# Performance work log

Hardware: AMD Instinct MI355X
Metric: run time of the kernel (lower is better)

Reference implementation:

```python
import jax, jax.numpy as jnp
import numpy as np

B, H, S, D = 2, 16, 2048, 64

def setup_inputs() -> dict:
    key = jax.random.key(0)
    kq, kk, kv = jax.random.split(key, 3)
    query = jax.random.normal(kq, (B, H, S, D), dtype=jnp.float32)
    k_ = jax.random.normal(kk, (B, H, S, D), dtype=jnp.float32)
    value = jax.random.normal(kv, (B, H, S, D), dtype=jnp.float32)
    # causal bool mask: True = masked (matches torch masked_fill semantics)
    attn_mask = jnp.triu(jnp.ones((S, S), dtype=bool), k=1)
    # no padding (all False) so no softmax row is fully masked
    key_padding_mask = jnp.zeros((B, S), dtype=bool)
    return {"query": query, "key": k_, "value": value,
            "attn_mask": attn_mask, "key_padding_mask": key_padding_mask}

def reference(query, key, value, attn_mask, key_padding_mask):
    scale = query.shape[-1] ** -0.5
    # [B,H,Sq,Sk] scores
    scores = jnp.einsum('bhqd,bhkd->bhqk', query, key) * scale
    scores = jnp.where(key_padding_mask[:, None, None, :], -jnp.inf, scores)
    scores = jnp.where(attn_mask, -jnp.inf, scores)
    attn = jax.nn.softmax(scores, axis=-1)
    # dropout=0.0 -> identity in eval/math
    return jnp.einsum('bhqk,bhkd->bhqd', attn, value)
```

## Files before the change

### kernel.cpp

```cpp
#include <hip/hip_runtime.h>
#include <hip/hip_bf16.h>


#define BHN 32
#define SEQ 2048
#define DIM 64
#define LSTR 72

typedef __attribute__((ext_vector_type(8)))  short    short8;
typedef __attribute__((ext_vector_type(4)))  short    short4v;
typedef __attribute__((ext_vector_type(4)))  float    float4v;
typedef __attribute__((ext_vector_type(16))) float    f32x16;
typedef __attribute__((ext_vector_type(4)))  unsigned uint4v;

__device__ __forceinline__ short f2b(float x) {
  __hip_bfloat16 h = __float2bfloat16(x);
  return __builtin_bit_cast(short, h);
}

__global__ __launch_bounds__(256) void prep_kernel(
    const float* __restrict__ K, const float* __restrict__ V,
    __hip_bfloat16* __restrict__ Kb, __hip_bfloat16* __restrict__ Vt) {
  __shared__ float t[64][65];
  const int bh = blockIdx.x, j = blockIdx.y, tid = threadIdx.x;
  const int r = tid >> 2, seg = (tid & 3) * 16;
  const size_t base = (size_t)bh * SEQ * DIM;
  {
    const float* ks = K + base + (size_t)(j * 64 + r) * DIM + seg;
    float4v k0 = *(const float4v*)(ks + 0);
    float4v k1 = *(const float4v*)(ks + 4);
    float4v k2 = *(const float4v*)(ks + 8);
    float4v k3 = *(const float4v*)(ks + 12);
    short8 a, b;
    a[0]=f2b(k0[0]); a[1]=f2b(k0[1]); a[2]=f2b(k0[2]); a[3]=f2b(k0[3]);
    a[4]=f2b(k1[0]); a[5]=f2b(k1[1]); a[6]=f2b(k1[2]); a[7]=f2b(k1[3]);
    b[0]=f2b(k2[0]); b[1]=f2b(k2[1]); b[2]=f2b(k2[2]); b[3]=f2b(k2[3]);
    b[4]=f2b(k3[0]); b[5]=f2b(k3[1]); b[6]=f2b(k3[2]); b[7]=f2b(k3[3]);
    __hip_bfloat16* kd = Kb + base + (size_t)(j * 64 + r) * DIM + seg;
    *(short8*)kd = a;
    *(short8*)(kd + 8) = b;
  }
  {
    const float* src = V + base + (size_t)(j * 64 + r) * DIM + seg;
    float4v f0 = *(const float4v*)(src + 0);
    float4v f1 = *(const float4v*)(src + 4);
    float4v f2 = *(const float4v*)(src + 8);
    float4v f3 = *(const float4v*)(src + 12);
    *(float4v*)&t[r][seg + 0]  = f0;
    *(float4v*)&t[r][seg + 4]  = f1;
    *(float4v*)&t[r][seg + 8]  = f2;
    *(float4v*)&t[r][seg + 12] = f3;
    __syncthreads();
    short8 n0, n1;
    #pragma unroll
    for (int i = 0; i < 4; ++i) {
      n0[i]     = f2b(t[seg + i][r]);
      n0[4 + i] = f2b(t[seg + 8 + i][r]);
      n1[i]     = f2b(t[seg + 4 + i][r]);
      n1[4 + i] = f2b(t[seg + 12 + i][r]);
    }
    __hip_bfloat16* dst = Vt + (size_t)bh * DIM * SEQ + (size_t)r * SEQ + j * 64 + seg;
    *(short8*)dst = n0;
    *(short8*)(dst + 8) = n1;
  }
}

__global__ __launch_bounds__(128) void fattn13(
    const float* __restrict__ Qg, const __hip_bfloat16* __restrict__ Kb,
    const __hip_bfloat16* __restrict__ Vt, float* __restrict__ Og) {
  __shared__ alignas(16) __hip_bfloat16 kt[2][64][LSTR];
  __shared__ alignas(16) __hip_bfloat16 vt[2][64][LSTR];

  const int bh    = blockIdx.x;
  const int qtile = 63 - blockIdx.y;
  const int tid   = threadIdx.x;
  const int w     = tid >> 6;
  const int lane  = tid & 63;
  const int l31   = lane & 31;
  const int hi    = lane >> 5;
  const int q0    = qtile * 32;
  const int jn    = (qtile >> 1) + 1;
  const int h     = jn >> 1;
  const int j0    = w ? h : 0;
  const int j1    = w ? jn : h;
  const size_t base  = (size_t)bh * SEQ * DIM;
  const size_t baseV = (size_t)bh * DIM * SEQ;

  const float QSCALE = 0.125f * 1.44269504088896340736f;

  short8 qf[4];
  {
    const float* qp = Qg + base + (size_t)(q0 + l31) * DIM + 8 * hi;
    #pragma unroll
    for (int s = 0; s < 4; ++s) {
      float4v f0 = *(const float4v*)(qp + 16 * s);
      float4v f1 = *(const float4v*)(qp + 16 * s + 4);
      short8 qv;
      qv[0] = f2b(f0[0] * QSCALE); qv[1] = f2b(f0[1] * QSCALE);
      qv[2] = f2b(f0[2] * QSCALE); qv[3] = f2b(f0[3] * QSCALE);
      qv[4] = f2b(f1[0] * QSCALE); qv[5] = f2b(f1[1] * QSCALE);
      qv[6] = f2b(f1[2] * QSCALE); qv[7] = f2b(f1[3] * QSCALE);
      qf[s] = qv;
    }
  }

  short8 ones;
  #pragma unroll
  for (int x = 0; x < 8; ++x) ones[x] = (short)0x3F80;

  f32x16 o0, o1, l16;
  #pragma unroll
  for (int i = 0; i < 16; ++i) { o0[i] = 0.f; o1[i] = 0.f; l16[i] = 0.f; }

  const int lr2 = lane >> 1;
  const int ch  = (lane & 1) * 32;

  short8 sk[8], sv[8];

  if (j0 < j1) {
    const int kb = 64 * j0;
    const __hip_bfloat16* kp0 = Kb + base + (size_t)(kb + lr2) * DIM + ch;
    const __hip_bfloat16* kp1 = Kb + base + (size_t)(kb + lr2 + 32) * DIM + ch;
    const __hip_bfloat16* vp0 = Vt + baseV + (size_t)lr2 * SEQ + kb + ch;
    const __hip_bfloat16* vp1 = Vt + baseV + (size_t)(lr2 + 32) * SEQ + kb + ch;
    #pragma unroll
    for (int i = 0; i < 4; ++i) {
      sk[i]     = *(const short8*)(kp0 + 8 * i);
      sk[4 + i] = *(const short8*)(kp1 + 8 * i);
      sv[i]     = *(const short8*)(vp0 + 8 * i);
      sv[4 + i] = *(const short8*)(vp1 + 8 * i);
    }
    #pragma unroll
    for (int i = 0; i < 4; ++i) {
      *(short8*)&kt[w][lr2][ch + 8 * i]      = sk[i];
      *(short8*)&kt[w][lr2 + 32][ch + 8 * i] = sk[4 + i];
      *(short8*)&vt[w][lr2][ch + 8 * i]      = sv[i];
      *(short8*)&vt[w][lr2 + 32][ch + 8 * i] = sv[4 + i];
    }
  }

  for (int j = j0; j < j1; ++j) {
    if (j + 1 < j1) {
      const int kb = (j + 1) * 64;
      const __hip_bfloat16* kp0 = Kb + base + (size_t)(kb + lr2) * DIM + ch;
      const __hip_bfloat16* kp1 = Kb + base + (size_t)(kb + lr2 + 32) * DIM + ch;
      #pragma unroll
      for (int i = 0; i < 4; ++i) {
        sk[i]     = *(const short8*)(kp0 + 8 * i);
        sk[4 + i] = *(const short8*)(kp1 + 8 * i);
      }
    }

    f32x16 p0, p1;
    #pragma unroll
    for (int i = 0; i < 16; ++i) { p0[i] = 0.f; p1[i] = 0.f; }
    __builtin_amdgcn_s_setprio(1);
    #pragma unroll
    for (int s = 0; s < 4; ++s) {
      short8 a0 = *(const short8*)&kt[w][l31][16 * s + 8 * hi];
      short8 a1 = *(const short8*)&kt[w][32 + l31][16 * s + 8 * hi];
      p0 = __builtin_amdgcn_mfma_f32_32x32x16_bf16(a0, qf[s], p0, 0, 0, 0);
      p1 = __builtin_amdgcn_mfma_f32_32x32x16_bf16(a1, qf[s], p1, 0, 0, 0);
    }
    __builtin_amdgcn_s_setprio(0);

    if (j == jn - 1) {
      const int qg  = q0 + l31;
      const int kb0 = 64 * j + 4 * hi;
      #pragma unroll
      for (int r = 0; r < 16; ++r) {
        const int kr = kb0 + (r & 3) + 8 * (r >> 2);
        if (kr > qg)      p0[r] = -1e30f;
        if (kr + 32 > qg) p1[r] = -1e30f;
      }
    }

    #pragma unroll
    for (int i = 0; i < 16; ++i) {
      p0[i] = __builtin_amdgcn_exp2f(p0[i]);
      p1[i] = __builtin_amdgcn_exp2f(p1[i]);
    }
    unsigned pw[16];
    #pragma unroll
    for (int i = 0; i < 8; ++i)
      asm("v_cvt_pk_bf16_f32 %0, %1, %2"
          : "=v"(pw[i]) : "v"(p0[2 * i]), "v"(p0[2 * i + 1]));
    #pragma unroll
    for (int i = 0; i < 8; ++i)
      asm("v_cvt_pk_bf16_f32 %0, %1, %2"
          : "=v"(pw[8 + i]) : "v"(p1[2 * i]), "v"(p1[2 * i + 1]));

    if (j + 1 < j1) {
      #pragma unroll
      for (int i = 0; i < 4; ++i) {
        *(short8*)&kt[w][lr2][ch + 8 * i]      = sk[i];
        *(short8*)&kt[w][lr2 + 32][ch + 8 * i] = sk[4 + i];
      }
      const int kb = (j + 1) * 64;
      const __hip_bfloat16* vp0 = Vt + baseV + (size_t)lr2 * SEQ + kb + ch;
      const __hip_bfloat16* vp1 = Vt + baseV + (size_t)(lr2 + 32) * SEQ + kb + ch;
      #pragma unroll
      for (int i = 0; i < 4; ++i) {
        sv[i]     = *(const short8*)(vp0 + 8 * i);
        sv[4 + i] = *(const short8*)(vp1 + 8 * i);
      }
    }

    __builtin_amdgcn_s_setprio(1);
    #pragma unroll
    for (int t = 0; t < 4; ++t) {
      uint4v u = {pw[4 * t], pw[4 * t + 1], pw[4 * t + 2], pw[4 * t + 3]};
      short8 pa = __builtin_bit_cast(short8, u);
      short8 b0 = *(const short8*)&vt[w][l31][16 * t + 8 * hi];
      short8 b1 = *(const short8*)&vt[w][32 + l31][16 * t + 8 * hi];
      o0  = __builtin_amdgcn_mfma_f32_32x32x16_bf16(pa, b0, o0, 0, 0, 0);
      o1  = __builtin_amdgcn_mfma_f32_32x32x16_bf16(pa, b1, o1, 0, 0, 0);
      l16 = __builtin_amdgcn_mfma_f32_32x32x16_bf16(pa, ones, l16, 0, 0, 0);
    }
    __builtin_amdgcn_s_setprio(0);

    if (j + 1 < j1) {
      #pragma unroll
      for (int i = 0; i < 4; ++i) {
        *(short8*)&vt[w][lr2][ch + 8 * i]      = sv[i];
        *(short8*)&vt[w][lr2 + 32][ch + 8 * i] = sv[4 + i];
      }
    }
  }

  __syncthreads();
  float* mb = (float*)&kt[0][0][0];
  if (w == 0) {
    #pragma unroll
    for (int r = 0; r < 16; ++r) {
      mb[lane * 49 + r]      = o0[r];
      mb[lane * 49 + 16 + r] = o1[r];
      mb[lane * 49 + 32 + r] = l16[r];
    }
  }
  __syncthreads();
  if (w == 1) {
    float* op = Og + base + (size_t)q0 * DIM + l31;
    #pragma unroll
    for (int r = 0; r < 16; ++r) {
      const float a0 = o0[r]  + mb[lane * 49 + r];
      const float a1 = o1[r]  + mb[lane * 49 + 16 + r];
      const float ll = l16[r] + mb[lane * 49 + 32 + r];
      const int row = (r & 3) + 8 * (r >> 2) + 4 * hi;
      const float iv = 1.0f / ll;
      op[(size_t)row * DIM]      = a0 * iv;
      op[(size_t)row * DIM + 32] = a1 * iv;
    }
  }
}

__global__ __launch_bounds__(256) void fattn_ref(
    const float* __restrict__ Qg, const float* __restrict__ Kg,
    const float* __restrict__ Vg, float* __restrict__ Og) {
  __shared__ alignas(16) __hip_bfloat16 kt[64][LSTR];
  __shared__ alignas(16) __hip_bfloat16 vt[64][LSTR];
  __shared__ alignas(16) __hip_bfloat16 pt[4][16][LSTR];

  const int bh   = blockIdx.x;
  const int qt   = gridDim.y - 1 - blockIdx.y;
  const int tid  = threadIdx.x;
  const int wave = tid >> 6;
  const int lane = tid & 63;
  const int ln   = lane & 15;
  const int quad = lane >> 4;
  const size_t base = (size_t)bh * SEQ * DIM;
  const int q0 = qt * 64;

  const float QSCALE = 0.125f * 1.44269504088896340736f;
  short8 qf[2];
  {
    const int qrow = q0 + wave * 16 + ln;
    const float* qp = Qg + base + (size_t)qrow * DIM + quad * 8;
    #pragma unroll
    for (int kk = 0; kk < 2; ++kk) {
      float4v f0 = *(const float4v*)(qp + kk * 32);
      float4v f1 = *(const float4v*)(qp + kk * 32 + 4);
      short8 qv;
      qv[0] = f2b(f0[0] * QSCALE); qv[1] = f2b(f0[1] * QSCALE);
      qv[2] = f2b(f0[2] * QSCALE); qv[3] = f2b(f0[3] * QSCALE);
      qv[4] = f2b(f1[0] * QSCALE); qv[5] = f2b(f1[1] * QSCALE);
      qv[6] = f2b(f1[2] * QSCALE); qv[7] = f2b(f1[3] * QSCALE);
      qf[kk] = qv;
    }
  }
  float4v o[4];
  #pragma unroll
  for (int dt = 0; dt < 4; ++dt) { float4v z = {0.f,0.f,0.f,0.f}; o[dt] = z; }
  float l_i[4] = {0.f, 0.f, 0.f, 0.f};

  for (int j = 0; j <= qt; ++j) {
    const int kbase = j * 64;
    __syncthreads();
    {
      const int r = tid >> 4, c = (tid & 15) * 4;
      #pragma unroll
      for (int it = 0; it < 4; ++it) {
        const int row = it * 16 + r;
        float4v f = *(const float4v*)(Kg + base + (size_t)(kbase + row) * DIM + c);
        short4v sv; sv[0]=f2b(f[0]); sv[1]=f2b(f[1]); sv[2]=f2b(f[2]); sv[3]=f2b(f[3]);
        *(short4v*)&kt[row][c] = sv;
      }
      const int d = tid & 63, s0 = (tid >> 6) * 4;
      #pragma unroll
      for (int it = 0; it < 4; ++it) {
        const int sk = it * 16 + s0;
        short4v sv;
        sv[0] = f2b(Vg[base + (size_t)(kbase + sk + 0) * DIM + d]);
        sv[1] = f2b(Vg[base + (size_t)(kbase + sk + 1) * DIM + d]);
        sv[2] = f2b(Vg[base + (size_t)(kbase + sk + 2) * DIM + d]);
        sv[3] = f2b(Vg[base + (size_t)(kbase + sk + 3) * DIM + d]);
        *(short4v*)&vt[d][sk] = sv;
      }
    }
    __syncthreads();

    float4v s[4];
    #pragma unroll
    for (int nt = 0; nt < 4; ++nt) {
      short8 b0 = *(const short8*)&kt[nt * 16 + ln][quad * 8];
      short8 b1 = *(const short8*)&kt[nt * 16 + ln][32 + quad * 8];
      float4v acc = {0.f,0.f,0.f,0.f};
      acc = __builtin_amdgcn_mfma_f32_16x16x32_bf16(qf[0], b0, acc, 0, 0, 0);
      acc = __builtin_amdgcn_mfma_f32_16x16x32_bf16(qf[1], b1, acc, 0, 0, 0);
      s[nt] = acc;
    }
    if (j == qt) {
      #pragma unroll
      for (int nt = 0; nt < 4; ++nt) {
        const int col = nt * 16 + ln;
        #pragma unroll
        for (int rg = 0; rg < 4; ++rg)
          if (col > wave * 16 + quad * 4 + rg) s[nt][rg] = -1e30f;
      }
    }
    #pragma unroll
    for (int rg = 0; rg < 4; ++rg) {
      float p0 = __builtin_amdgcn_exp2f(s[0][rg]);
      float p1 = __builtin_amdgcn_exp2f(s[1][rg]);
      float p2 = __builtin_amdgcn_exp2f(s[2][rg]);
      float p3 = __builtin_amdgcn_exp2f(s[3][rg]);
      s[0][rg]=p0; s[1][rg]=p1; s[2][rg]=p2; s[3][rg]=p3;
      float rs = (p0 + p1) + (p2 + p3);
      rs += __shfl_xor(rs, 1, 64); rs += __shfl_xor(rs, 2, 64);
      rs += __shfl_xor(rs, 4, 64); rs += __shfl_xor(rs, 8, 64);
      l_i[rg] += rs;
    }
    #pragma unroll
    for (int nt = 0; nt < 4; ++nt)
      #pragma unroll
      for (int rg = 0; rg < 4; ++rg)
        pt[wave][quad * 4 + rg][nt * 16 + ln] = __float2bfloat16(s[nt][rg]);
    short8 pa0 = *(const short8*)&pt[wave][ln][quad * 8];
    short8 pa1 = *(const short8*)&pt[wave][ln][32 + quad * 8];
    #pragma unroll
    for (int dt = 0; dt < 4; ++dt) {
      short8 vb0 = *(const short8*)&vt[dt * 16 + ln][quad * 8];
      short8 vb1 = *(const short8*)&vt[dt * 16 + ln][32 + quad * 8];
      o[dt] = __builtin_amdgcn_mfma_f32_16x16x32_bf16(pa0, vb0, o[dt], 0, 0, 0);
      o[dt] = __builtin_amdgcn_mfma_f32_16x16x32_bf16(pa1, vb1, o[dt], 0, 0, 0);
    }
  }
  #pragma unroll
  for (int rg = 0; rg < 4; ++rg) {
    const float inv = 1.0f / l_i[rg];
    const int row = q0 + wave * 16 + quad * 4 + rg;
    float* op = Og + base + (size_t)row * DIM + ln;
    #pragma unroll
    for (int dt = 0; dt < 4; ++dt) op[dt * 16] = o[dt][rg] * inv;
  }
}

extern "C" void kernel_launch(void* const* d_in, const int* in_sizes, int n_in,
                              void* d_out, int out_size, void* d_ws, size_t ws_size,
                              hipStream_t stream) {
  (void)in_sizes; (void)n_in; (void)out_size;
  const float* Q = (const float*)d_in[0];
  const float* K = (const float*)d_in[1];
  const float* V = (const float*)d_in[2];
  float* O = (float*)d_out;
  const size_t need = (size_t)2 * BHN * SEQ * DIM * sizeof(__hip_bfloat16);
  if (ws_size >= need) {
    __hip_bfloat16* Kb = (__hip_bfloat16*)d_ws;
    __hip_bfloat16* Vt = Kb + (size_t)BHN * SEQ * DIM;
    prep_kernel<<<dim3(BHN, SEQ / 64), 256, 0, stream>>>(K, V, Kb, Vt);
    fattn13<<<dim3(BHN, 64), 128, 0, stream>>>(Q, Kb, Vt, O);
  } else {
    fattn_ref<<<dim3(BHN, SEQ / 64), 256, 0, stream>>>(Q, K, V, O);
  }
}
```

Before: 151.2 us.

## Halve key block to 32 to trim causal padding and shrink LDS footprint

Switches the attention kernel's key/value tile from 64 to 32 keys, so the number of key tiles per 32-row query tile becomes qtile+1 instead of (qtile/2)+1. Only the final diagonal tile is partly masked, so less masked work is computed. LDS for K and V is halved, and the cross-wave reduction is split into three staged passes through a smaller buffer. In exchange there are twice as many loop iterations with less MFMA work each, plus extra syncthreads in the epilogue.

```diff
diff --git a/kernel.cpp b/kernel.cpp
--- a/kernel.cpp
+++ b/kernel.cpp
@@ -5,7 +5,9 @@
 #define BHN 32
 #define SEQ 2048
 #define DIM 64
+#define KBLK 32
 #define LSTR 72
+#define VSTR 36
 
 typedef __attribute__((ext_vector_type(8)))  short    short8;
 typedef __attribute__((ext_vector_type(4)))  short    short4v;
@@ -65,11 +67,11 @@
   }
 }
 
-__global__ __launch_bounds__(128) void fattn13(
+__global__ __launch_bounds__(128) void fattn15(
     const float* __restrict__ Qg, const __hip_bfloat16* __restrict__ Kb,
     const __hip_bfloat16* __restrict__ Vt, float* __restrict__ Og) {
-  __shared__ alignas(16) __hip_bfloat16 kt[2][64][LSTR];
-  __shared__ alignas(16) __hip_bfloat16 vt[2][64][LSTR];
+  __shared__ alignas(16) __hip_bfloat16 kt[2][KBLK][LSTR];
+  __shared__ alignas(16) __hip_bfloat16 vtl[2][64][VSTR];
 
   const int bh    = blockIdx.x;
   const int qtile = 63 - blockIdx.y;
@@ -79,10 +81,10 @@
   const int l31   = lane & 31;
   const int hi    = lane >> 5;
   const int q0    = qtile * 32;
-  const int jn    = (qtile >> 1) + 1;
-  const int h     = jn >> 1;
+  const int tn    = qtile + 1;
+  const int h     = tn >> 1;
   const int j0    = w ? h : 0;
-  const int j1    = w ? jn : h;
+  const int j1    = w ? tn : h;
   const size_t base  = (size_t)bh * SEQ * DIM;
   const size_t baseV = (size_t)bh * DIM * SEQ;
 
@@ -112,107 +114,81 @@
   #pragma unroll
   for (int i = 0; i < 16; ++i) { o0[i] = 0.f; o1[i] = 0.f; l16[i] = 0.f; }
 
-  const int lr2 = lane >> 1;
-  const int ch  = (lane & 1) * 32;
-
-  short8 sk[8], sv[8];
+  const int srow = lane >> 1;
+  const int ch   = (lane & 1) * 32;
+
+  short8 sk[4], sv[4];
 
   if (j0 < j1) {
-    const int kb = 64 * j0;
-    const __hip_bfloat16* kp0 = Kb + base + (size_t)(kb + lr2) * DIM + ch;
-    const __hip_bfloat16* kp1 = Kb + base + (size_t)(kb + lr2 + 32) * DIM + ch;
-    const __hip_bfloat16* vp0 = Vt + baseV + (size_t)lr2 * SEQ + kb + ch;
-    const __hip_bfloat16* vp1 = Vt + baseV + (size_t)(lr2 + 32) * SEQ + kb + ch;
+    const int kb = KBLK * j0;
+    const __hip_bfloat16* kp = Kb + base + (size_t)(kb + srow) * DIM + ch;
+    const __hip_bfloat16* vp = Vt + baseV + (size_t)lane * SEQ + kb;
     #pragma unroll
     for (int i = 0; i < 4; ++i) {
-      sk[i]     = *(const short8*)(kp0 + 8 * i);
-      sk[4 + i] = *(const short8*)(kp1 + 8 * i);
-      sv[i]     = *(const short8*)(vp0 + 8 * i);
-      sv[4 + i] = *(const short8*)(vp1 + 8 * i);
+      sk[i] = *(const short8*)(kp + 8 * i);
+      sv[i] = *(const short8*)(vp + 8 * i);
     }
     #pragma unroll
     for (int i = 0; i < 4; ++i) {
-      *(short8*)&kt[w][lr2][ch + 8 * i]      = sk[i];
-      *(short8*)&kt[w][lr2 + 32][ch + 8 * i] = sk[4 + i];
-      *(short8*)&vt[w][lr2][ch + 8 * i]      = sv[i];
-      *(short8*)&vt[w][lr2 + 32][ch + 8 * i] = sv[4 + i];
+      *(short8*)&kt[w][srow][ch + 8 * i] = sk[i];
+      *(short8*)&vtl[w][lane][8 * i]     = sv[i];
     }
   }
 
   for (int j = j0; j < j1; ++j) {
+    const int kb = KBLK * j;
+
     if (j + 1 < j1) {
-      const int kb = (j + 1) * 64;
-      const __hip_bfloat16* kp0 = Kb + base + (size_t)(kb + lr2) * DIM + ch;
-      const __hip_bfloat16* kp1 = Kb + base + (size_t)(kb + lr2 + 32) * DIM + ch;
-      #pragma unroll
-      for (int i = 0; i < 4; ++i) {
-        sk[i]     = *(const short8*)(kp0 + 8 * i);
-        sk[4 + i] = *(const short8*)(kp1 + 8 * i);
-      }
-    }
-
-    f32x16 p0, p1;
-    #pragma unroll
-    for (int i = 0; i < 16; ++i) { p0[i] = 0.f; p1[i] = 0.f; }
+      const __hip_bfloat16* kp = Kb + base + (size_t)(kb + KBLK + srow) * DIM + ch;
+      #pragma unroll
+      for (int i = 0; i < 4; ++i) sk[i] = *(const short8*)(kp + 8 * i);
+    }
+
+    f32x16 p0;
+    #pragma unroll
+    for (int i = 0; i < 16; ++i) p0[i] = 0.f;
     __builtin_amdgcn_s_setprio(1);
     #pragma unroll
     for (int s = 0; s < 4; ++s) {
       short8 a0 = *(const short8*)&kt[w][l31][16 * s + 8 * hi];
-      short8 a1 = *(const short8*)&kt[w][32 + l31][16 * s + 8 * hi];
       p0 = __builtin_amdgcn_mfma_f32_32x32x16_bf16(a0, qf[s], p0, 0, 0, 0);
-      p1 = __builtin_amdgcn_mfma_f32_32x32x16_bf16(a1, qf[s], p1, 0, 0, 0);
     }
     __builtin_amdgcn_s_setprio(0);
 
-    if (j == jn - 1) {
+    if (j == tn - 1) {
       const int qg  = q0 + l31;
-      const int kb0 = 64 * j + 4 * hi;
+      const int kb0 = kb + 4 * hi;
       #pragma unroll
       for (int r = 0; r < 16; ++r) {
         const int kr = kb0 + (r & 3) + 8 * (r >> 2);
-        if (kr > qg)      p0[r] = -1e30f;
-        if (kr + 32 > qg) p1[r] = -1e30f;
+        if (kr > qg) p0[r] = -1e30f;
       }
     }
 
     #pragma unroll
-    for (int i = 0; i < 16; ++i) {
-      p0[i] = __builtin_amdgcn_exp2f(p0[i]);
-      p1[i] = __builtin_amdgcn_exp2f(p1[i]);
-    }
-    unsigned pw[16];
+    for (int i = 0; i < 16; ++i) p0[i] = __builtin_amdgcn_exp2f(p0[i]);
+    unsigned pw[8];
     #pragma unroll
     for (int i = 0; i < 8; ++i)
       asm("v_cvt_pk_bf16_f32 %0, %1, %2"
           : "=v"(pw[i]) : "v"(p0[2 * i]), "v"(p0[2 * i + 1]));
-    #pragma unroll
-    for (int i = 0; i < 8; ++i)
-      asm("v_cvt_pk_bf16_f32 %0, %1, %2"
-          : "=v"(pw[8 + i]) : "v"(p1[2 * i]), "v"(p1[2 * i + 1]));
 
     if (j + 1 < j1) {
       #pragma unroll
-      for (int i = 0; i < 4; ++i) {
-        *(short8*)&kt[w][lr2][ch + 8 * i]      = sk[i];
-        *(short8*)&kt[w][lr2 + 32][ch + 8 * i] = sk[4 + i];
-      }
-      const int kb = (j + 1) * 64;
-      const __hip_bfloat16* vp0 = Vt + baseV + (size_t)lr2 * SEQ + kb + ch;
-      const __hip_bfloat16* vp1 = Vt + baseV + (size_t)(lr2 + 32) * SEQ + kb + ch;
-      #pragma unroll
-      for (int i = 0; i < 4; ++i) {
-        sv[i]     = *(const short8*)(vp0 + 8 * i);
-        sv[4 + i] = *(const short8*)(vp1 + 8 * i);
-      }
+      for (int i = 0; i < 4; ++i)
+        *(short8*)&kt[w][srow][ch + 8 * i] = sk[i];
+      const __hip_bfloat16* vp = Vt + baseV + (size_t)lane * SEQ + kb + KBLK;
+      #pragma unroll
+      for (int i = 0; i < 4; ++i) sv[i] = *(const short8*)(vp + 8 * i);
     }
 
     __builtin_amdgcn_s_setprio(1);
     #pragma unroll
-    for (int t = 0; t < 4; ++t) {
+    for (int t = 0; t < 2; ++t) {
       uint4v u = {pw[4 * t], pw[4 * t + 1], pw[4 * t + 2], pw[4 * t + 3]};
       short8 pa = __builtin_bit_cast(short8, u);
-      short8 b0 = *(const short8*)&vt[w][l31][16 * t + 8 * hi];
-      short8 b1 = *(const short8*)&vt[w][32 + l31][16 * t + 8 * hi];
+      short8 b0 = *(const short8*)&vtl[w][l31][16 * t + 8 * hi];
+      short8 b1 = *(const short8*)&vtl[w][32 + l31][16 * t + 8 * hi];
       o0  = __builtin_amdgcn_mfma_f32_32x32x16_bf16(pa, b0, o0, 0, 0, 0);
       o1  = __builtin_amdgcn_mfma_f32_32x32x16_bf16(pa, b1, o1, 0, 0, 0);
       l16 = __builtin_amdgcn_mfma_f32_32x32x16_bf16(pa, ones, l16, 0, 0, 0);
@@ -221,35 +197,47 @@
 
     if (j + 1 < j1) {
       #pragma unroll
-      for (int i = 0; i < 4; ++i) {
-        *(short8*)&vt[w][lr2][ch + 8 * i]      = sv[i];
-        *(short8*)&vt[w][lr2 + 32][ch + 8 * i] = sv[4 + i];
-      }
-    }
-  }
-
-  __syncthreads();
+      for (int i = 0; i < 4; ++i)
+        *(short8*)&vtl[w][lane][8 * i] = sv[i];
+    }
+  }
+
   float* mb = (float*)&kt[0][0][0];
+  __syncthreads();
   if (w == 0) {
     #pragma unroll
-    for (int r = 0; r < 16; ++r) {
-      mb[lane * 49 + r]      = o0[r];
-      mb[lane * 49 + 16 + r] = o1[r];
-      mb[lane * 49 + 32 + r] = l16[r];
-    }
+    for (int r = 0; r < 16; ++r) mb[lane * 17 + r] = o0[r];
+  }
+  __syncthreads();
+  if (w == 1) {
+    #pragma unroll
+    for (int r = 0; r < 16; ++r) o0[r] += mb[lane * 17 + r];
+  }
+  __syncthreads();
+  if (w == 0) {
+    #pragma unroll
+    for (int r = 0; r < 16; ++r) mb[lane * 17 + r] = o1[r];
+  }
+  __syncthreads();
+  if (w == 1) {
+    #pragma unroll
+    for (int r = 0; r < 16; ++r) o1[r] += mb[lane * 17 + r];
+  }
+  __syncthreads();
+  if (w == 0) {
+    #pragma unroll
+    for (int r = 0; r < 16; ++r) mb[lane * 17 + r] = l16[r];
   }
   __syncthreads();
   if (w == 1) {
     float* op = Og + base + (size_t)q0 * DIM + l31;
     #pragma unroll
     for (int r = 0; r < 16; ++r) {
-      const float a0 = o0[r]  + mb[lane * 49 + r];
-      const float a1 = o1[r]  + mb[lane * 49 + 16 + r];
-      const float ll = l16[r] + mb[lane * 49 + 32 + r];
+      const float ll = l16[r] + mb[lane * 17 + r];
       const int row = (r & 3) + 8 * (r >> 2) + 4 * hi;
       const float iv = 1.0f / ll;
-      op[(size_t)row * DIM]      = a0 * iv;
-      op[(size_t)row * DIM + 32] = a1 * iv;
+      op[(size_t)row * DIM]      = o0[r] * iv;
+      op[(size_t)row * DIM + 32] = o1[r] * iv;
     }
   }
 }
@@ -388,7 +376,7 @@
     __hip_bfloat16* Kb = (__hip_bfloat16*)d_ws;
     __hip_bfloat16* Vt = Kb + (size_t)BHN * SEQ * DIM;
     prep_kernel<<<dim3(BHN, SEQ / 64), 256, 0, stream>>>(K, V, Kb, Vt);
-    fattn13<<<dim3(BHN, 64), 128, 0, stream>>>(Q, Kb, Vt, O);
+    fattn15<<<dim3(BHN, 64), 128, 0, stream>>>(Q, Kb, Vt, O);
   } else {
     fattn_ref<<<dim3(BHN, SEQ / 64), 256, 0, stream>>>(Q, K, V, O);
   }
```

Measured after the change: 160.8 us. 6.4% more time.
